# Optimization experiments

Hardware: AMD Instinct MI355X
Metric: run time of the kernel (lower is better)

## Reference

```python
import jax, jax.numpy as jnp
import numpy as np
from jax import lax

B, C, H, W = 4, 64, 96, 320
RC = C // 4                     # reduced channels = 16
D = 48                          # max_disp = len(norm_disp_range)
NORM_DISP = jnp.arange(D, dtype=jnp.float32) / 160.0
EPS = 1e-5


def conv2d(x, w, b=None, pad=0, groups=1):
    y = lax.conv_general_dilated(x, w, (1, 1), ((pad, pad), (pad, pad)),
                                 dimension_numbers=('NCHW', 'OIHW', 'NCHW'),
                                 feature_group_count=groups)
    if b is not None:
        y = y + b[None, :, None, None]
    return y


def group_norm(x, g, b, groups=8):
    n, c, h, w = x.shape
    xg = x.reshape(n, groups, c // groups, h, w)
    mu = xg.mean(axis=(2, 3, 4), keepdims=True)
    var = xg.var(axis=(2, 3, 4), keepdims=True)
    xn = ((xg - mu) * lax.rsqrt(var + EPS)).reshape(n, c, h, w)
    return xn * g[None, :, None, None] + b[None, :, None, None]


elu = jax.nn.elu


def setup_inputs() -> dict:
    key = jax.random.key(0)
    ks = iter(jax.random.split(key, 32))

    def rn(shape, scale=0.05):
        return jax.random.normal(next(ks), shape, dtype=jnp.float32) * scale

    inp = {
        'left_feat': jax.random.normal(next(ks), (B, C, H, W), jnp.float32),
        'right_feat': jax.random.normal(next(ks), (B, C, H, W), jnp.float32),
        'directs': jnp.ones((B,), jnp.float32),
        # q_conv / k_conv: 1x1 conv (no bias) + GroupNorm(8) params
        'qw': rn((RC, C, 1, 1)), 'q_g': jnp.ones((RC,)), 'q_b': jnp.zeros((RC,)),
        'kw': rn((RC, C, 1, 1)), 'k_g': jnp.ones((RC,)), 'k_b': jnp.zeros((RC,)),
        # global_attn: avgpool -> 1x1 (rc->rc/2) -> ELU -> 1x1 (rc/2->rc)
        'ga_w1': rn((RC // 2, RC, 1, 1)), 'ga_b1': jnp.zeros((RC // 2,)),
        'ga_w2': rn((RC, RC // 2, 1, 1)), 'ga_b2': jnp.zeros((RC,)),
        # local_attn: 3x3 conv + GN(8) + ELU
        'la_w': rn((RC, RC, 3, 3)), 'la_b': jnp.zeros((RC,)),
        'la_g': jnp.ones((RC,)), 'la_bb': jnp.zeros((RC,)),
        # attn_fusion: 1x1 (2rc->rc) -> ELU -> 1x1 (rc->D)
        'af_w1': rn((RC, 2 * RC, 1, 1)), 'af_b1': jnp.zeros((RC,)),
        'af_w2': rn((D, RC, 1, 1)), 'af_b2': jnp.zeros((D,)),
        # refine_cost: depthwise 3x3 (groups=D) -> ELU -> 1x1
        'rdw_w': rn((D, 1, 3, 3)), 'rdw_b': jnp.zeros((D,)),
        'rpw_w': rn((D, D, 1, 1)), 'rpw_b': jnp.zeros((D,)),
        # fusion: reflection-pad 3x3 conv (C+D -> C) + SELayer(C, 16)
        'fu_w': rn((C, C + D, 3, 3)), 'fu_b': jnp.zeros((C,)),
        'se_w1': rn((C // 16, C)), 'se_w2': rn((C, C // 16)),
    }
    return inp


def reference(left_feat, right_feat, directs, qw, q_g, q_b, kw, k_g, k_b,
              ga_w1, ga_b1, ga_w2, ga_b2, la_w, la_b, la_g, la_bb,
              af_w1, af_b1, af_w2, af_b2, rdw_w, rdw_b, rpw_w, rpw_b,
              fu_w, fu_b, se_w1, se_w2):
    q = elu(group_norm(conv2d(left_feat, qw), q_g, q_b))      # [B,RC,H,W]
    k = elu(group_norm(conv2d(right_feat, kw), k_g, k_b))     # [B,RC,H,W]

    gp = q.mean(axis=(2, 3), keepdims=True)                   # AdaptiveAvgPool2d(1)
    gfeat = conv2d(elu(conv2d(gp, ga_w1, ga_b1)), ga_w2, ga_b2)
    gfeat = jnp.broadcast_to(gfeat, q.shape)
    lfeat = elu(group_norm(conv2d(q, la_w, la_b, pad=1), la_g, la_bb))
    comb = jnp.concatenate([gfeat, lfeat], axis=1)            # [B,2RC,H,W]
    attn = conv2d(elu(conv2d(comb, af_w1, af_b1)), af_w2, af_b2)  # [B,D,H,W]

    # Warped cost volume. grid_sample shifts only the x-coordinate by
    # disp*2*directs (normalized, align_corners=True), i.e. a constant
    # horizontal shift of disp*directs*(W-1) pixels with border clamping.
    # Channel-mean commutes with horizontal bilinear sampling, so warp
    # the channel-mean map directly (identical math, D x less work).
    km = k.mean(axis=1)                                       # [B,H,W]
    shift = NORM_DISP[None, :] * directs[:, None] * (W - 1)   # [B,D]
    pos = jnp.arange(W, dtype=jnp.float32)[None, None, :] + shift[:, :, None]  # [B,D,W]
    x0 = jnp.floor(pos)
    f = pos - x0                                              # bilinear frac
    i0 = jnp.clip(x0, 0, W - 1).astype(jnp.int32)
    i1 = jnp.clip(x0 + 1, 0, W - 1).astype(jnp.int32)

    def gather(idx):  # km[b,h,idx[b,d,w]] -> [B,D,H,W]
        return jnp.take_along_axis(
            km[:, None, :, :],
            jnp.broadcast_to(idx[:, :, None, :], (B, D, H, W)), axis=3)

    fw = f[:, :, None, :]
    warped = gather(i0) * (1.0 - fw) + gather(i1) * fw        # [B,D,H,W]
    vol = warped * jax.nn.sigmoid(attn)                       # sigmoid-weighted volume

    cost = conv2d(elu(conv2d(vol, rdw_w, rdw_b, pad=1, groups=D)), rpw_w, rpw_b)
    norm_cost = jax.nn.softmax(cost, axis=1)

    # fusion: ReflectionPad2d(1) + 3x3 conv, SE layer, ELU
    cat = jnp.concatenate([left_feat, norm_cost], axis=1)     # [B,C+D,H,W]
    cat_p = jnp.pad(cat, ((0, 0), (0, 0), (1, 1), (1, 1)), mode='reflect')
    fused = conv2d(cat_p, fu_w, fu_b)                         # [B,C,H,W]
    y = fused.mean(axis=(2, 3))                               # [B,C]
    y = jax.nn.sigmoid(jax.nn.relu(y @ se_w1.T) @ se_w2.T)
    x = elu(fused * y[:, :, None, None])
    return (x, norm_cost)
```

## Files before the change

kernel.cpp:

```cpp
#include <hip/hip_runtime.h>
#include <math.h>

static constexpr int B_  = 4;
static constexpr int C_  = 64;
static constexpr int H_  = 96;
static constexpr int W_  = 320;
static constexpr int HW  = H_ * W_;
static constexpr int RCH = 16;
static constexpr int D_  = 48;
static constexpr int NG  = 8;
static constexpr int CPG = RCH / NG;
static constexpr float EPS_ = 1e-5f;
static constexpr int APX = 322;

typedef __attribute__((ext_vector_type(8))) short short8;
typedef __attribute__((ext_vector_type(4))) float f32x4;
typedef __attribute__((ext_vector_type(4))) unsigned int u32x4;

__device__ __forceinline__ float elu1(float x) { return x > 0.f ? x : __expf(x) - 1.f; }
__device__ __forceinline__ float sigm(float x) { return 1.f / (1.f + __expf(-x)); }
__device__ __forceinline__ unsigned bf16rne(float f) {
    unsigned u = __builtin_bit_cast(unsigned, f);
    u += 0x7fffu + ((u >> 16) & 1u);
    return u >> 16;
}
__device__ __forceinline__ void gload16(const void* g, void* l) {
    __builtin_amdgcn_global_load_lds((const __attribute__((address_space(1))) unsigned int*)g,
                                     (__attribute__((address_space(3))) unsigned int*)l, 16, 0, 0);
}

__global__ __launch_bounds__(256) void k_wrepack(
    const float* __restrict__ qw, const float* __restrict__ kw, const float* __restrict__ law,
    float* __restrict__ qwp, float* __restrict__ kwp, float* __restrict__ lawp)
{
    int t = threadIdx.x;
    for (int i = t; i < RCH * C_; i += 256) {
        int c = i >> 4, r = i & 15;
        qwp[i] = qw[r * C_ + c];
        kwp[i] = kw[r * C_ + c];
    }
    for (int i = t; i < RCH * RCH * 9; i += 256) {
        int co = i & 15, rest = i >> 4;
        int ci = rest / 9, tap = rest % 9;
        lawp[i] = law[(co * RCH + ci) * 9 + tap];
    }
}

__global__ __launch_bounds__(256) void k_conv_qk(
    const float* __restrict__ left, const float* __restrict__ right,
    const float* __restrict__ qwp, const float* __restrict__ kwp,
    float* __restrict__ qraw, float* __restrict__ kraw)
{
    int idx = blockIdx.x * 256 + threadIdx.x;
    int half = idx / (B_ * HW / 2);
    int r0 = idx - half * (B_ * HW / 2);
    int b = r0 / (HW / 2), p2 = r0 - b * (HW / 2);
    int p = p2 * 2;
    const float* src = (half ? right : left) + (size_t)b * C_ * HW + p;
    const float* wp  = half ? kwp : qwp;
    float* dst = (half ? kraw : qraw) + (size_t)b * RCH * HW + p;
    float2 acc[RCH];
#pragma unroll
    for (int r = 0; r < RCH; r++) acc[r] = make_float2(0.f, 0.f);
#pragma unroll
    for (int c = 0; c < C_; c++) {
        float2 v = *reinterpret_cast<const float2*>(src + (size_t)c * HW);
        const float* wrow = wp + c * RCH;
#pragma unroll
        for (int r = 0; r < RCH; r++) {
            acc[r].x += v.x * wrow[r];
            acc[r].y += v.y * wrow[r];
        }
    }
#pragma unroll
    for (int r = 0; r < RCH; r++)
        *reinterpret_cast<float2*>(dst + (size_t)r * HW) = acc[r];
}

__global__ __launch_bounds__(256) void k_gn_stats2(const float* __restrict__ qsrc,
    const float* __restrict__ ksrc, float* __restrict__ stats)
{
    int z = blockIdx.x;
    const float* src = (z < 32) ? qsrc : ksrc;
    int zz = (z < 32) ? z : z - 32;
    int b = zz / NG, g = zz % NG;
    const float4* base = (const float4*)(src + ((size_t)b * RCH + g * CPG) * HW);
    float s = 0.f, ss = 0.f;
    for (int i = threadIdx.x; i < CPG * HW / 4; i += 256) {
        float4 v = base[i];
        s  += v.x + v.y + v.z + v.w;
        ss += v.x * v.x + v.y * v.y + v.z * v.z + v.w * v.w;
    }
    __shared__ float rs[256], rq[256];
    rs[threadIdx.x] = s; rq[threadIdx.x] = ss; __syncthreads();
    for (int off = 128; off > 0; off >>= 1) {
        if (threadIdx.x < off) { rs[threadIdx.x] += rs[threadIdx.x + off]; rq[threadIdx.x] += rq[threadIdx.x + off]; }
        __syncthreads();
    }
    if (threadIdx.x == 0) {
        float inv = 1.f / (float)(CPG * HW);
        float m = rs[0] * inv;
        float var = rq[0] * inv - m * m;
        stats[z * 2 + 0] = m;
        stats[z * 2 + 1] = rsqrtf(var + EPS_);
    }
}

__global__ __launch_bounds__(256) void k_gn_stats(const float* __restrict__ src, float* __restrict__ stats)
{
    int b = blockIdx.x / NG, g = blockIdx.x % NG;
    const float4* base = (const float4*)(src + ((size_t)b * RCH + g * CPG) * HW);
    float s = 0.f, ss = 0.f;
    for (int i = threadIdx.x; i < CPG * HW / 4; i += 256) {
        float4 v = base[i];
        s  += v.x + v.y + v.z + v.w;
        ss += v.x * v.x + v.y * v.y + v.z * v.z + v.w * v.w;
    }
    __shared__ float rs[256], rq[256];
    rs[threadIdx.x] = s; rq[threadIdx.x] = ss; __syncthreads();
    for (int off = 128; off > 0; off >>= 1) {
        if (threadIdx.x < off) { rs[threadIdx.x] += rs[threadIdx.x + off]; rq[threadIdx.x] += rq[threadIdx.x + off]; }
        __syncthreads();
    }
    if (threadIdx.x == 0) {
        float inv = 1.f / (float)(CPG * HW);
        float m = rs[0] * inv;
        float var = rq[0] * inv - m * m;
        stats[blockIdx.x * 2 + 0] = m;
        stats[blockIdx.x * 2 + 1] = rsqrtf(var + EPS_);
    }
}

__global__ __launch_bounds__(256) void k_gn_apply(float* __restrict__ x, const float* __restrict__ stats,
    const float* __restrict__ gam, const float* __restrict__ bet)
{
    int idx4 = blockIdx.x * 256 + threadIdx.x;
    int b = idx4 / (RCH * HW / 4);
    int rc = (idx4 / (HW / 4)) % RCH;
    int g = rc >> 1;
    float m = stats[(b * NG + g) * 2], is = stats[(b * NG + g) * 2 + 1];
    float ga = gam[rc] * is, be = bet[rc] - m * is * gam[rc];
    float4 v = ((const float4*)x)[idx4];
    v.x = elu1(v.x * ga + be); v.y = elu1(v.y * ga + be);
    v.z = elu1(v.z * ga + be); v.w = elu1(v.w * ga + be);
    ((float4*)x)[idx4] = v;
}

__global__ __launch_bounds__(256) void k_km(const float* __restrict__ kraw, const float* __restrict__ stats,
    const float* __restrict__ gam, const float* __restrict__ bet, float* __restrict__ km)
{
    int idx = blockIdx.x * 256 + threadIdx.x;
    int b = idx / HW, p = idx - b * HW;
    float s = 0.f;
#pragma unroll
    for (int rc = 0; rc < RCH; rc++) {
        int g = rc >> 1;
        float m = stats[(b * NG + g) * 2], is = stats[(b * NG + g) * 2 + 1];
        float v = (kraw[((size_t)b * RCH + rc) * HW + p] - m) * is * gam[rc] + bet[rc];
        s += elu1(v);
    }
    km[idx] = s * (1.f / (float)RCH);
}

__global__ __launch_bounds__(256) void k_rowmean(const float* __restrict__ src, float* __restrict__ out)
{
    const float4* base = (const float4*)(src + (size_t)blockIdx.x * HW);
    float s = 0.f;
    for (int p = threadIdx.x; p < HW / 4; p += 256) {
        float4 v = base[p];
        s += v.x + v.y + v.z + v.w;
    }
    __shared__ float red[256];
    red[threadIdx.x] = s; __syncthreads();
    for (int off = 128; off > 0; off >>= 1) {
        if (threadIdx.x < off) red[threadIdx.x] += red[threadIdx.x + off];
        __syncthreads();
    }
    if (threadIdx.x == 0) out[blockIdx.x] = red[0] * (1.f / (float)HW);
}

__global__ __launch_bounds__(64) void k_gfeat(const float* __restrict__ gp,
    const float* __restrict__ gaw1, const float* __restrict__ gab1,
    const float* __restrict__ gaw2, const float* __restrict__ gab2,
    const float* __restrict__ afw1, const float* __restrict__ afb1,
    float* __restrict__ gbias)
{
    __shared__ float g1[B_ * 8], gf[B_ * RCH];
    int t = threadIdx.x;
    if (t < B_ * 8) {
        int b = t >> 3, o = t & 7;
        float a = gab1[o];
        for (int i = 0; i < RCH; i++) a += gaw1[o * RCH + i] * gp[b * RCH + i];
        g1[b * 8 + o] = elu1(a);
    }
    __syncthreads();
    {
        int b = t >> 4, o = t & 15;
        float a = gab2[o];
        for (int i = 0; i < 8; i++) a += gaw2[o * 8 + i] * g1[b * 8 + i];
        gf[t] = a;
    }
    __syncthreads();
    {
        int b = t >> 4, o = t & 15;
        float a = afb1[o];
        for (int i = 0; i < RCH; i++) a += afw1[o * 2 * RCH + i] * gf[b * RCH + i];
        gbias[t] = a;
    }
}

__global__ __launch_bounds__(256) void k_conv_la(const float* __restrict__ q,
    const float* __restrict__ lawp, const float* __restrict__ lab, float* __restrict__ lraw)
{
    int idx = blockIdx.x * 256 + threadIdx.x;
    int b = idx / HW, p = idx - b * HW;
    int h = p / W_, w = p - h * W_;
    float acc[RCH];
#pragma unroll
    for (int co = 0; co < RCH; co++) acc[co] = lab[co];
#pragma unroll
    for (int ci = 0; ci < RCH; ci++) {
        const float* qb = q + ((size_t)b * RCH + ci) * HW;
#pragma unroll
        for (int kh = 0; kh < 3; kh++) {
            int hh = h + kh - 1;
            if (hh < 0 || hh >= H_) continue;
            float a0 = (w - 1 >= 0) ? qb[hh * W_ + w - 1] : 0.f;
            float a1 = qb[hh * W_ + w];
            float a2 = (w + 1 < W_) ? qb[hh * W_ + w + 1] : 0.f;
            const float* wp0 = lawp + (ci * 9 + kh * 3) * RCH;
#pragma unroll
            for (int co = 0; co < RCH; co++)
                acc[co] += a0 * wp0[co] + a1 * wp0[RCH + co] + a2 * wp0[2 * RCH + co];
        }
    }
#pragma unroll
    for (int co = 0; co < RCH; co++) lraw[((size_t)b * RCH + co) * HW + p] = acc[co];
}

__global__ __launch_bounds__(320) void k_vol(const float* __restrict__ lraw,
    const float* __restrict__ stats, const float* __restrict__ lg, const float* __restrict__ lb,
    const float* __restrict__ gbias, const float* __restrict__ afw1,
    const float* __restrict__ afw2, const float* __restrict__ afb2,
    const float* __restrict__ km, const float* __restrict__ directs, float* __restrict__ vol)
{
    __shared__ float w1[RCH * 2 * RCH];
    __shared__ float w2[D_ * RCH];
    __shared__ float b2[D_];
    __shared__ float kms[W_];
    int blk = blockIdx.x;
    int b = blk / H_, h = blk - b * H_;
    int t = threadIdx.x;
    for (int i = t; i < RCH * 2 * RCH; i += 320) w1[i] = afw1[i];
    for (int i = t; i < D_ * RCH; i += 320) w2[i] = afw2[i];
    if (t < D_) b2[t] = afb2[t];
    kms[t] = km[(size_t)b * HW + h * W_ + t];
    __syncthreads();
    int w = t, p = h * W_ + w;
    float lf[RCH];
#pragma unroll
    for (int rc = 0; rc < RCH; rc++) {
        int g = rc >> 1;
        float m = stats[(b * NG + g) * 2], is = stats[(b * NG + g) * 2 + 1];
        lf[rc] = elu1((lraw[((size_t)b * RCH + rc) * HW + p] - m) * is * lg[rc] + lb[rc]);
    }
    float hid[RCH];
#pragma unroll
    for (int o = 0; o < RCH; o++) {
        float a = gbias[b * RCH + o];
#pragma unroll
        for (int i = 0; i < RCH; i++) a += w1[o * 2 * RCH + RCH + i] * lf[i];
        hid[o] = elu1(a);
    }
    float dir = directs[b];
    for (int d = 0; d < D_; d++) {
        float a = b2[d];
#pragma unroll
        for (int o = 0; o < RCH; o++) a += w2[d * RCH + o] * hid[o];
        float s = sigm(a);
        float shift = ((float)d / 160.f) * dir * (float)(W_ - 1);
        float pos = (float)w + shift;
        float x0 = floorf(pos);
        float f = pos - x0;
        float c0 = fminf(fmaxf(x0, 0.f), (float)(W_ - 1));
        float c1 = fminf(fmaxf(x0 + 1.f, 0.f), (float)(W_ - 1));
        int i0 = (int)c0, i1 = (int)c1;
        float wv = kms[i0] * (1.f - f) + kms[i1] * f;
        vol[((size_t)(b * D_ + d)) * HW + p] = wv * s;
    }
}

__global__ __launch_bounds__(256) void k_dw(const float* __restrict__ vol,
    const float* __restrict__ wgt, const float* __restrict__ bias, float* __restrict__ dwout)
{
    int idx = blockIdx.x * 256 + threadIdx.x;
    int p4 = idx % (HW / 4);
    int d  = (idx / (HW / 4)) % D_;
    int b  = idx / (D_ * HW / 4);
    int h = p4 / (W_ / 4), w = (p4 % (W_ / 4)) * 4;
    const float* vb = vol + ((size_t)(b * D_ + d)) * HW;
    float wz[9];
#pragma unroll
    for (int i = 0; i < 9; i++) wz[i] = wgt[d * 9 + i];
    float bv = bias[d];
    float acc[4] = {bv, bv, bv, bv};
#pragma unroll
    for (int r = 0; r < 3; r++) {
        int hh = h + r - 1;
        if (hh < 0 || hh >= H_) continue;
        const float* row = vb + hh * W_;
        float4 c = *(const float4*)(row + w);
        float in6[6];
        in6[0] = (w > 0) ? row[w - 1] : 0.f;
        in6[1] = c.x; in6[2] = c.y; in6[3] = c.z; in6[4] = c.w;
        in6[5] = (w + 4 < W_) ? row[w + 4] : 0.f;
#pragma unroll
        for (int j = 0; j < 4; j++)
            acc[j] += in6[j] * wz[r * 3] + in6[j + 1] * wz[r * 3 + 1] + in6[j + 2] * wz[r * 3 + 2];
    }
    float4 o;
    o.x = elu1(acc[0]); o.y = elu1(acc[1]); o.z = elu1(acc[2]); o.w = elu1(acc[3]);
    ((float4*)dwout)[idx] = o;
}

__global__ __launch_bounds__(256) void k_prep(const float* __restrict__ left, unsigned int* __restrict__ abf)
{
    int idx = blockIdx.x * 256 + threadIdx.x;
    int px = idx % APX;
    int bh = idx / APX;
    int b = bh / H_, h = bh % H_;
    int w = px - 1;
    w = w < 0 ? -w : (w >= W_ ? 2 * W_ - 2 - w : w);
    const float* src = left + (size_t)b * C_ * HW + h * W_ + w;
    unsigned int* dst = abf + (size_t)idx * 60;
#pragma unroll
    for (int q4 = 0; q4 < 8; q4++) {
        u32x4 t;
#pragma unroll
        for (int z = 0; z < 4; z++) {
            int ci = (q4 * 4 + z) * 2;
            float f0 = src[(size_t)ci * HW];
            float f1 = src[(size_t)(ci + 1) * HW];
            t[z] = bf16rne(f0) | (bf16rne(f1) << 16);
        }
        *reinterpret_cast<u32x4*>(dst + q4 * 4) = t;
    }
    *reinterpret_cast<u32x4*>(dst + 56) = (u32x4){0u, 0u, 0u, 0u};
}

__global__ __launch_bounds__(256) void k_rpw(float* __restrict__ ncost,
    const float* __restrict__ wgt, const float* __restrict__ bias,
    unsigned int* __restrict__ abf)
{
    __shared__ float wr[D_ * D_];
    __shared__ float bs[D_];
    for (int i = threadIdx.x; i < D_ * D_; i += 256) wr[i] = wgt[i];
    if (threadIdx.x < D_) bs[threadIdx.x] = bias[threadIdx.x];
    __syncthreads();
    int idx = blockIdx.x * 256 + threadIdx.x;
    int b = idx / HW, p = idx - b * HW;
    int h = p / W_, w = p - h * W_;
    float v[D_];
#pragma unroll
    for (int i = 0; i < D_; i++) v[i] = ncost[((size_t)(b * D_ + i)) * HW + p];
    float cst[D_];
    float mx = -1e30f;
#pragma unroll
    for (int d = 0; d < D_; d++) {
        float a = bs[d];
        const float4* wrow = (const float4*)&wr[d * D_];
#pragma unroll
        for (int i4 = 0; i4 < D_ / 4; i4++) {
            float4 wv = wrow[i4];
            a += wv.x * v[i4 * 4 + 0] + wv.y * v[i4 * 4 + 1]
               + wv.z * v[i4 * 4 + 2] + wv.w * v[i4 * 4 + 3];
        }
        cst[d] = a; mx = fmaxf(mx, a);
    }
    float s = 0.f;
#pragma unroll
    for (int d = 0; d < D_; d++) { float e = __expf(cst[d] - mx); cst[d] = e; s += e; }
    float inv = 1.f / s;
#pragma unroll
    for (int d = 0; d < D_; d++) {
        cst[d] *= inv;
        ncost[((size_t)(b * D_ + d)) * HW + p] = cst[d];
    }
    u32x4 pk[6];
#pragma unroll
    for (int q4 = 0; q4 < 6; q4++)
#pragma unroll
        for (int z = 0; z < 4; z++) {
            int d = (q4 * 4 + z) * 2;
            pk[q4][z] = bf16rne(cst[d]) | (bf16rne(cst[d + 1]) << 16);
        }
    size_t bh322 = (size_t)(b * H_ + h) * APX;
    unsigned int* dst = abf + (bh322 + (w + 1)) * 60 + 32;
#pragma unroll
    for (int q4 = 0; q4 < 6; q4++) *reinterpret_cast<u32x4*>(dst + q4 * 4) = pk[q4];
    if (w == 1 || w == W_ - 2) {
        unsigned int* dst2 = abf + (bh322 + (w == 1 ? 0 : APX - 1)) * 60 + 32;
#pragma unroll
        for (int q4 = 0; q4 < 6; q4++) *reinterpret_cast<u32x4*>(dst2 + q4 * 4) = pk[q4];
    }
}

__global__ __launch_bounds__(256) void k_wpack(const float* __restrict__ fw, unsigned short* __restrict__ wpack,
    float* __restrict__ ymean)
{
    int bi = blockIdx.x;
    int t = threadIdx.x;
    if (bi == 0 && t < B_ * C_) ymean[t] = 0.f;
    int tap = bi >> 2, kblk = bi & 3;
    int kh = tap / 3, kw2 = tap % 3;
    int ct = t >> 6, l = t & 63;
    int co = ct * 16 + (l & 15);
    int ci0 = kblk * 32 + ((l >> 4) & 3) * 8;
    unsigned short v[8];
#pragma unroll
    for (int j = 0; j < 8; j++) {
        int ci = ci0 + j;
        float f = (ci < 112) ? fw[((size_t)(co * 112 + ci)) * 9 + kh * 3 + kw2] : 0.f;
        v[j] = (unsigned short)bf16rne(f);
    }
    *reinterpret_cast<short8*>(wpack + ((size_t)bi * 256 + t) * 8) = *reinterpret_cast<short8*>(v);
}

static constexpr int LROWB  = 240;
static constexpr int LPLANB = 66 * LROWB;
__global__ __launch_bounds__(256, 1) void k_fused_mfma(
    const unsigned int* __restrict__ abf,
    const unsigned short* __restrict__ wpack, const float* __restrict__ fb,
    float* __restrict__ fused, float* __restrict__ ymean)
{
    __shared__ __align__(16) unsigned int Atile4[15844];
    int bb = blockIdx.z;
    int h0 = blockIdx.y * 2;
    int w0 = blockIdx.x * 64;
    int tid = threadIdx.x;
    int wid = tid >> 6;
    int l   = tid & 63;

    {
        int hh = h0 - 1 + wid;
        hh = hh < 0 ? -hh : (hh >= H_ ? 2 * H_ - 2 - hh : hh);
        const char* gsrc = (const char*)(abf + ((size_t)(bb * H_ + hh) * APX + w0) * 60);
        char* lbase = (char*)Atile4 + wid * LPLANB;
#pragma unroll
        for (int i = 0; i < 15; i++)
            gload16(gsrc + (i * 64 + l) * 16, lbase + i * 1024);
        if (l < 30) gload16(gsrc + (960 + l) * 16, lbase + 15 * 1024);
    }
    __syncthreads();

    int row = wid >> 1;
    int ch  = wid & 1;
    int li = l & 15, lg = l >> 4;

    const short8* __restrict__ wp8 = reinterpret_cast<const short8*>(wpack);

    f32x4 acc[4][2];
    float bv0 = fb[(ch * 2 + 0) * 16 + li];
    float bv1 = fb[(ch * 2 + 1) * 16 + li];
#pragma unroll
    for (int pt = 0; pt < 4; pt++) {
        acc[pt][0] = (f32x4){bv0, bv0, bv0, bv0};
        acc[pt][1] = (f32x4){bv1, bv1, bv1, bv1};
    }

    const char* Abase = (const char*)Atile4;
#pragma unroll
    for (int kh = 0; kh < 3; kh++) {
#pragma unroll
        for (int kw2 = 0; kw2 < 3; kw2++) {
#pragma unroll
            for (int kblk = 0; kblk < 4; kblk++) {
                int step = (kh * 3 + kw2) * 4 + kblk;
                short8 b0 = wp8[step * 256 + (ch * 2 + 0) * 64 + l];
                short8 b1 = wp8[step * 256 + (ch * 2 + 1) * 64 + l];
                int rbase = (row + kh) * LPLANB + kblk * 64 + lg * 16 + (kw2 + li) * LROWB;
#pragma unroll
                for (int pt = 0; pt < 4; pt++) {
                    short8 a = *reinterpret_cast<const short8*>(Abase + rbase + pt * (16 * LROWB));
                    acc[pt][0] = __builtin_amdgcn_mfma_f32_16x16x32_bf16(a, b0, acc[pt][0], 0, 0, 0);
                    acc[pt][1] = __builtin_amdgcn_mfma_f32_16x16x32_bf16(a, b1, acc[pt][1], 0, 0, 0);
                }
            }
        }
    }

    int h = h0 + row;
#pragma unroll
    for (int j = 0; j < 2; j++) {
        int co = (ch * 2 + j) * 16 + li;
        float* ob = fused + ((size_t)(bb * C_ + co) * H_ + h) * W_ + w0 + lg * 4;
#pragma unroll
        for (int pt = 0; pt < 4; pt++) {
            *reinterpret_cast<f32x4*>(ob + pt * 16) = acc[pt][j];
        }
    }
    float s0 = 0.f, s1 = 0.f;
#pragma unroll
    for (int pt = 0; pt < 4; pt++)
#pragma unroll
        for (int rg = 0; rg < 4; rg++) { s0 += acc[pt][0][rg]; s1 += acc[pt][1][rg]; }
    s0 += __shfl_xor(s0, 16); s0 += __shfl_xor(s0, 32);
    s1 += __shfl_xor(s1, 16); s1 += __shfl_xor(s1, 32);
    if (lg == 0) {
        atomicAdd(&ymean[bb * C_ + (ch * 2 + 0) * 16 + li], s0);
        atomicAdd(&ymean[bb * C_ + (ch * 2 + 1) * 16 + li], s1);
    }
}

__global__ __launch_bounds__(256) void k_se(const float* __restrict__ ymean,
    const float* __restrict__ w1, const float* __restrict__ w2, float* __restrict__ scale)
{
    __shared__ float h4[B_ * 4];
    int t = threadIdx.x;
    const float invHW = 1.f / (float)HW;
    if (t < B_ * 4) {
        int b = t >> 2, o = t & 3;
        float a = 0.f;
        for (int c = 0; c < C_; c++) a += w1[o * C_ + c] * (ymean[b * C_ + c] * invHW);
        h4[b * 4 + o] = fmaxf(a, 0.f);
    }
    __syncthreads();
    {
        int b = t >> 6, c = t & 63;
        float a = 0.f;
        for (int o = 0; o < 4; o++) a += w2[c * 4 + o] * h4[b * 4 + o];
        scale[t] = sigm(a);
    }
}

__global__ __launch_bounds__(256) void k_final(const float* __restrict__ fused,
    const float* __restrict__ scale, float* __restrict__ out)
{
    int idx4 = blockIdx.x * 256 + threadIdx.x;
    int bc = idx4 / (HW / 4);
    float sc = scale[bc];
    float4 v = ((const float4*)fused)[idx4];
    v.x = elu1(v.x * sc); v.y = elu1(v.y * sc);
    v.z = elu1(v.z * sc); v.w = elu1(v.w * sc);
    ((float4*)out)[idx4] = v;
}

extern "C" void kernel_launch(void* const* d_in, const int* in_sizes, int n_in,
                              void* d_out, int out_size, void* d_ws, size_t ws_size,
                              hipStream_t stream)
{
    const float* left   = (const float*)d_in[0];
    const float* right  = (const float*)d_in[1];
    const float* directs= (const float*)d_in[2];
    const float* qw     = (const float*)d_in[3];
    const float* q_g    = (const float*)d_in[4];
    const float* q_b    = (const float*)d_in[5];
    const float* kw     = (const float*)d_in[6];
    const float* k_g    = (const float*)d_in[7];
    const float* k_b    = (const float*)d_in[8];
    const float* gaw1   = (const float*)d_in[9];
    const float* gab1   = (const float*)d_in[10];
    const float* gaw2   = (const float*)d_in[11];
    const float* gab2   = (const float*)d_in[12];
    const float* law    = (const float*)d_in[13];
    const float* lab    = (const float*)d_in[14];
    const float* lag    = (const float*)d_in[15];
    const float* labb   = (const float*)d_in[16];
    const float* afw1   = (const float*)d_in[17];
    const float* afb1   = (const float*)d_in[18];
    const float* afw2   = (const float*)d_in[19];
    const float* afb2   = (const float*)d_in[20];
    const float* rdww   = (const float*)d_in[21];
    const float* rdwb   = (const float*)d_in[22];
    const float* rpww   = (const float*)d_in[23];
    const float* rpwb   = (const float*)d_in[24];
    const float* fuw    = (const float*)d_in[25];
    const float* fub    = (const float*)d_in[26];
    const float* sew1   = (const float*)d_in[27];
    const float* sew2   = (const float*)d_in[28];

    float* ws    = (float*)d_ws;
    float* qraw  = ws + 0;
    float* kraw  = ws + 1966080;
    float* km    = ws + 3932160;
    float* vol   = ws + 9953280;
    float* smal  = ws + 15851520;
    unsigned int* abf = (unsigned int*)(ws + 0);
    float* fused = ws + 7418880;
    float* lraw  = kraw;
    unsigned short* wpack = (unsigned short*)(ws + 15811584);

    float* qwp   = ws + 4055040;
    float* kwp   = ws + 4056064;
    float* lawp  = ws + 4057088;

    float* stQ   = smal + 0;
    float* stL   = smal + 128;
    float* gp    = smal + 192;
    float* gbias = smal + 256;
    float* ymean = smal + 320;
    float* scal  = smal + 576;

    float* xout  = (float*)d_out;
    float* ncost = xout + 7864320;

    k_wrepack<<<1, 256, 0, stream>>>(qw, kw, law, qwp, kwp, lawp);
    k_conv_qk<<<480, 256, 0, stream>>>(left, right, qwp, kwp, qraw, kraw);
    k_gn_stats2<<<64, 256, 0, stream>>>(qraw, kraw, stQ);
    k_gn_apply<<<1920, 256, 0, stream>>>(qraw, stQ, q_g, q_b);
    k_km<<<480, 256, 0, stream>>>(kraw, stQ + 64, k_g, k_b, km);
    k_rowmean<<<64, 256, 0, stream>>>(qraw, gp);
    k_gfeat<<<1, 64, 0, stream>>>(gp, gaw1, gab1, gaw2, gab2, afw1, afb1, gbias);
    k_conv_la<<<480, 256, 0, stream>>>(qraw, lawp, lab, lraw);
    k_gn_stats<<<32, 256, 0, stream>>>(lraw, stL);
    k_vol<<<384, 320, 0, stream>>>(lraw, stL, lag, labb, gbias, afw1, afw2, afb2, km, directs, vol);
    k_dw<<<5760, 256, 0, stream>>>(vol, rdww, rdwb, ncost);
    k_prep<<<483, 256, 0, stream>>>(left, abf);
    k_rpw<<<480, 256, 0, stream>>>(ncost, rpww, rpwb, abf);
    k_wpack<<<36, 256, 0, stream>>>(fuw, wpack, ymean);
    k_fused_mfma<<<dim3(5, 48, 4), 256, 0, stream>>>(abf, wpack, fub, fused, ymean);
    k_se<<<1, 256, 0, stream>>>(ymean, sew1, sew2, scal);
    k_final<<<7680, 256, 0, stream>>>(fused, scal, xout);
}
```

Before: 262.0 us.

## Widen fused conv tile to 80 pixels, remap blocks, prefetch weight fragments

The fused 3x3 MFMA conv now covers 80 pixels per block instead of 64, so the grid shrinks from 960 to 768 blocks and each weight fragment is reused across five pixel tiles. A flat block index is permuted so that consecutive blocks spread across the (h,b) space. The weight-fragment loads for the next K-step are software-prefetched, and all A fragments for a step are loaded before its MFMAs are issued. This raises register and LDS use per block, which may lower occupancy, and 768 blocks may fill the CUs less evenly.

```diff
diff --git a/kernel.cpp b/kernel.cpp
--- a/kernel.cpp
+++ b/kernel.cpp
@@ -426,17 +426,22 @@
     *reinterpret_cast<short8*>(wpack + ((size_t)bi * 256 + t) * 8) = *reinterpret_cast<short8*>(v);
 }
 
+static constexpr int TPX    = 80;
+static constexpr int LPXC   = TPX + 2;
 static constexpr int LROWB  = 240;
-static constexpr int LPLANB = 66 * LROWB;
+static constexpr int LPLANB = LPXC * LROWB;
+static constexpr int NPT    = TPX / 16;
 __global__ __launch_bounds__(256, 1) void k_fused_mfma(
     const unsigned int* __restrict__ abf,
     const unsigned short* __restrict__ wpack, const float* __restrict__ fb,
     float* __restrict__ fused, float* __restrict__ ymean)
 {
-    __shared__ __align__(16) unsigned int Atile4[15844];
-    int bb = blockIdx.z;
-    int h0 = blockIdx.y * 2;
-    int w0 = blockIdx.x * 64;
+    __shared__ __align__(16) unsigned int Atile4[4 * LPXC * 60 + 4];
+    int flat = blockIdx.x + 4 * (blockIdx.y + 48 * blockIdx.z);
+    int tau = (flat & 7) * 96 + (flat >> 3);
+    int wx = tau & 3, hy = (tau >> 2) % 48, bb = tau / 192;
+    int h0 = hy * 2;
+    int w0 = wx * TPX;
     int tid = threadIdx.x;
     int wid = tid >> 6;
     int l   = tid & 63;
@@ -447,9 +452,9 @@
         const char* gsrc = (const char*)(abf + ((size_t)(bb * H_ + hh) * APX + w0) * 60);
         char* lbase = (char*)Atile4 + wid * LPLANB;
 #pragma unroll
-        for (int i = 0; i < 15; i++)
+        for (int i = 0; i < 19; i++)
             gload16(gsrc + (i * 64 + l) * 16, lbase + i * 1024);
-        if (l < 30) gload16(gsrc + (960 + l) * 16, lbase + 15 * 1024);
+        if (l < 14) gload16(gsrc + (1216 + l) * 16, lbase + 1216 * 16);
     }
     __syncthreads();
 
@@ -459,34 +464,37 @@
 
     const short8* __restrict__ wp8 = reinterpret_cast<const short8*>(wpack);
 
-    f32x4 acc[4][2];
+    f32x4 acc[NPT][2];
     float bv0 = fb[(ch * 2 + 0) * 16 + li];
     float bv1 = fb[(ch * 2 + 1) * 16 + li];
 #pragma unroll
-    for (int pt = 0; pt < 4; pt++) {
+    for (int pt = 0; pt < NPT; pt++) {
         acc[pt][0] = (f32x4){bv0, bv0, bv0, bv0};
         acc[pt][1] = (f32x4){bv1, bv1, bv1, bv1};
     }
 
     const char* Abase = (const char*)Atile4;
-#pragma unroll
-    for (int kh = 0; kh < 3; kh++) {
-#pragma unroll
-        for (int kw2 = 0; kw2 < 3; kw2++) {
-#pragma unroll
-            for (int kblk = 0; kblk < 4; kblk++) {
-                int step = (kh * 3 + kw2) * 4 + kblk;
-                short8 b0 = wp8[step * 256 + (ch * 2 + 0) * 64 + l];
-                short8 b1 = wp8[step * 256 + (ch * 2 + 1) * 64 + l];
-                int rbase = (row + kh) * LPLANB + kblk * 64 + lg * 16 + (kw2 + li) * LROWB;
-#pragma unroll
-                for (int pt = 0; pt < 4; pt++) {
-                    short8 a = *reinterpret_cast<const short8*>(Abase + rbase + pt * (16 * LROWB));
-                    acc[pt][0] = __builtin_amdgcn_mfma_f32_16x16x32_bf16(a, b0, acc[pt][0], 0, 0, 0);
-                    acc[pt][1] = __builtin_amdgcn_mfma_f32_16x16x32_bf16(a, b1, acc[pt][1], 0, 0, 0);
-                }
-            }
-        }
+    short8 bc0 = wp8[0 * 256 + (ch * 2 + 0) * 64 + l];
+    short8 bc1 = wp8[0 * 256 + (ch * 2 + 1) * 64 + l];
+#pragma unroll
+    for (int step = 0; step < 36; step++) {
+        int kh = step / 12, kw2 = (step / 4) % 3, kblk = step & 3;
+        short8 bn0 = bc0, bn1 = bc1;
+        if (step < 35) {
+            bn0 = wp8[(step + 1) * 256 + (ch * 2 + 0) * 64 + l];
+            bn1 = wp8[(step + 1) * 256 + (ch * 2 + 1) * 64 + l];
+        }
+        int rbase = (row + kh) * LPLANB + kblk * 64 + lg * 16 + (kw2 + li) * LROWB;
+        short8 av[NPT];
+#pragma unroll
+        for (int pt = 0; pt < NPT; pt++)
+            av[pt] = *reinterpret_cast<const short8*>(Abase + rbase + pt * (16 * LROWB));
+#pragma unroll
+        for (int pt = 0; pt < NPT; pt++) {
+            acc[pt][0] = __builtin_amdgcn_mfma_f32_16x16x32_bf16(av[pt], bc0, acc[pt][0], 0, 0, 0);
+            acc[pt][1] = __builtin_amdgcn_mfma_f32_16x16x32_bf16(av[pt], bc1, acc[pt][1], 0, 0, 0);
+        }
+        bc0 = bn0; bc1 = bn1;
     }
 
     int h = h0 + row;
@@ -495,13 +503,13 @@
         int co = (ch * 2 + j) * 16 + li;
         float* ob = fused + ((size_t)(bb * C_ + co) * H_ + h) * W_ + w0 + lg * 4;
 #pragma unroll
-        for (int pt = 0; pt < 4; pt++) {
+        for (int pt = 0; pt < NPT; pt++) {
             *reinterpret_cast<f32x4*>(ob + pt * 16) = acc[pt][j];
         }
     }
     float s0 = 0.f, s1 = 0.f;
 #pragma unroll
-    for (int pt = 0; pt < 4; pt++)
+    for (int pt = 0; pt < NPT; pt++)
 #pragma unroll
         for (int rg = 0; rg < 4; rg++) { s0 += acc[pt][0][rg]; s1 += acc[pt][1][rg]; }
     s0 += __shfl_xor(s0, 16); s0 += __shfl_xor(s0, 32);
@@ -618,7 +626,7 @@
     k_prep<<<483, 256, 0, stream>>>(left, abf);
     k_rpw<<<480, 256, 0, stream>>>(ncost, rpww, rpwb, abf);
     k_wpack<<<36, 256, 0, stream>>>(fuw, wpack, ymean);
-    k_fused_mfma<<<dim3(5, 48, 4), 256, 0, stream>>>(abf, wpack, fub, fused, ymean);
+    k_fused_mfma<<<dim3(4, 48, 4), 256, 0, stream>>>(abf, wpack, fub, fused, ymean);
     k_se<<<1, 256, 0, stream>>>(ymean, sew1, sew2, scal);
     k_final<<<7680, 256, 0, stream>>>(fused, scal, xout);
 }
```

New measurement: 248.9 us. 5.0% less time.
